# Kernel tuning notes

Hardware: AMD Instinct MI355X
Metric: run time of the kernel (lower is better)

Reference implementation:

```python
import jax, jax.numpy as jnp
import numpy as np

N = 2_000_000
REL_DIM = 14
CAN_DIM = 64
N_TYPES = 4


def setup_inputs() -> dict:
    key = jax.random.key(0)
    ka, kb, kia, kib, kw, kbias = jax.random.split(key, 6)
    return {
        "relation_logits_a": jax.random.normal(ka, (N, REL_DIM), dtype=jnp.float32),
        "relation_logits_b": jax.random.normal(kb, (N, REL_DIM), dtype=jnp.float32),
        "frame_type_ids_a": jax.random.randint(kia, (N,), 0, N_TYPES, dtype=jnp.int32),
        "frame_type_ids_b": jax.random.randint(kib, (N,), 0, N_TYPES, dtype=jnp.int32),
        # stacked expert params: W[e] is (REL_DIM, CAN_DIM), b[e] is (CAN_DIM,)
        "W": jax.random.normal(kw, (N_TYPES, REL_DIM, CAN_DIM), dtype=jnp.float32) * 0.26,
        "b": jax.random.normal(kbias, (N_TYPES, CAN_DIM), dtype=jnp.float32) * 0.26,
    }


def _batch_project(x, ids, W, b):
    # x: (N, REL_DIM), ids: (N,) int in [0, N_TYPES)
    # Masked dispatch to 4 tiny linear experts; peak intermediate is (N, CAN_DIM).
    out = jnp.zeros((x.shape[0], CAN_DIM), dtype=x.dtype)
    for e in range(N_TYPES):
        y = x @ W[e] + b[e]                      # (N, CAN_DIM)
        out = out + jnp.where((ids == e)[:, None], y, jnp.zeros((), x.dtype))
    return out


def reference(relation_logits_a, relation_logits_b, frame_type_ids_a, frame_type_ids_b, W, b):
    proj_a = _batch_project(relation_logits_a, frame_type_ids_a, W, b)
    proj_b = _batch_project(relation_logits_b, frame_type_ids_b, W, b)
    # F.mse_loss default reduction='mean'
    diff = proj_a - proj_b
    return jnp.mean(diff * diff)
```

## Files before the change

kernel.cpp:

```cpp
#include <hip/hip_runtime.h>
#include <hip/hip_bf16.h>
#include <hip/hip_fp16.h>


#define N_ROWS   2000000
#define CHUNK    64
#define N_CHUNKS (N_ROWS / CHUNK)
#define LDSP     72

typedef _Float16       h8  __attribute__((ext_vector_type(8)));
typedef float          f4  __attribute__((ext_vector_type(4)));
typedef unsigned short us8 __attribute__((ext_vector_type(8)));

__device__ __forceinline__ unsigned short f2h_bits(float x) {
    return __builtin_bit_cast(unsigned short, (_Float16)x);
}

__global__ void __launch_bounds__(64)
frame_loss_mfma(const float* __restrict__ A, const float* __restrict__ B,
                const int* __restrict__ IDA, const int* __restrict__ IDB,
                const float* __restrict__ W, const float* __restrict__ BIAS,
                float* __restrict__ out)
{
    __shared__ unsigned short sA[CHUNK * LDSP];
    __shared__ unsigned short sB[CHUNK * LDSP];

    const int lane = threadIdx.x & 63;
    const int sub  = lane & 15;
    const int quad = lane >> 4;

    h8 wf[8], nwf[8];
#pragma unroll
    for (int ct = 0; ct < 4; ++ct) {
#pragma unroll
        for (int s = 0; s < 2; ++s) {
            const int c = ct * 16 + sub;
            us8 bits;
#pragma unroll
            for (int j = 0; j < 8; ++j) {
                const int k = s * 32 + quad * 8 + j;
                float v = 0.0f;
                if (k < 56) {
                    const int e = k / 14;
                    const int kk = k - e * 14;
                    v = W[(e * 14 + kk) * 64 + c];
                } else if (k < 60) {
                    v = BIAS[(k - 56) * 64 + c];
                }
                bits[j] = f2h_bits(v);
            }
            wf[ct * 2 + s] = __builtin_bit_cast(h8, bits);
            us8 nb = bits ^ (unsigned short)0x8000;
            nwf[ct * 2 + s] = __builtin_bit_cast(h8, nb);
        }
    }

    float lsum = 0.0f;
    unsigned int* const rowA32 = (unsigned int*)(sA + lane * LDSP);
    unsigned int* const rowB32 = (unsigned int*)(sB + lane * LDSP);

    for (int chunk = blockIdx.x; chunk < N_CHUNKS; chunk += gridDim.x) {
        const int row = chunk * CHUNK + lane;
        const float2* ap = (const float2*)(A + (size_t)row * 14);
        const float2* bp = (const float2*)(B + (size_t)row * 14);
        float2 av[7], bv[7];
#pragma unroll
        for (int t = 0; t < 7; ++t) av[t] = ap[t];
#pragma unroll
        for (int t = 0; t < 7; ++t) bv[t] = bp[t];
        const int ea = IDA[row];
        const int eb = IDB[row];

        const us8 z = {0, 0, 0, 0, 0, 0, 0, 0};
#pragma unroll
        for (int t = 0; t < 9; ++t) ((us8*)rowA32)[t] = z;
#pragma unroll
        for (int t = 0; t < 9; ++t) ((us8*)rowB32)[t] = z;

#pragma unroll
        for (int t = 0; t < 7; ++t)
            rowA32[7 * ea + t] = (unsigned)f2h_bits(av[t].x) | ((unsigned)f2h_bits(av[t].y) << 16);
        rowA32[28 + (ea >> 1)] = 0x3C00u << (16 * (ea & 1));
#pragma unroll
        for (int t = 0; t < 7; ++t)
            rowB32[7 * eb + t] = (unsigned)f2h_bits(bv[t].x) | ((unsigned)f2h_bits(bv[t].y) << 16);
        rowB32[28 + (eb >> 1)] = 0x3C00u << (16 * (eb & 1));

        __syncthreads();

#pragma unroll
        for (int t = 0; t < 4; ++t) {
            const unsigned short* fa = sA + (t * 16 + sub) * LDSP + quad * 8;
            const unsigned short* fb = sB + (t * 16 + sub) * LDSP + quad * 8;
            h8 a0 = __builtin_bit_cast(h8, *(const us8*)fa);
            h8 a1 = __builtin_bit_cast(h8, *(const us8*)(fa + 32));
            h8 b0 = __builtin_bit_cast(h8, *(const us8*)fb);
            h8 b1 = __builtin_bit_cast(h8, *(const us8*)(fb + 32));
#pragma unroll
            for (int ct = 0; ct < 4; ++ct) {
                f4 acc = {0.0f, 0.0f, 0.0f, 0.0f};
                acc = __builtin_amdgcn_mfma_f32_16x16x32_f16(a0, wf[ct * 2 + 0], acc, 0, 0, 0);
                acc = __builtin_amdgcn_mfma_f32_16x16x32_f16(a1, wf[ct * 2 + 1], acc, 0, 0, 0);
                acc = __builtin_amdgcn_mfma_f32_16x16x32_f16(b0, nwf[ct * 2 + 0], acc, 0, 0, 0);
                acc = __builtin_amdgcn_mfma_f32_16x16x32_f16(b1, nwf[ct * 2 + 1], acc, 0, 0, 0);
                lsum += acc[0] * acc[0] + acc[1] * acc[1] + acc[2] * acc[2] + acc[3] * acc[3];
            }
        }
        __syncthreads();
    }

#pragma unroll
    for (int off = 32; off > 0; off >>= 1)
        lsum += __shfl_down(lsum, off, 64);
    if (lane == 0)
        atomicAdd(out, lsum * (1.0f / 128000000.0f));
}

extern "C" void kernel_launch(void* const* d_in, const int* in_sizes, int n_in,
                              void* d_out, int out_size, void* d_ws, size_t ws_size,
                              hipStream_t stream) {
    const float* A    = (const float*)d_in[0];
    const float* B    = (const float*)d_in[1];
    const int*   IDA  = (const int*)d_in[2];
    const int*   IDB  = (const int*)d_in[3];
    const float* W    = (const float*)d_in[4];
    const float* BIAS = (const float*)d_in[5];
    float* out = (float*)d_out;

    hipMemsetAsync(out, 0, sizeof(float), stream);
    frame_loss_mfma<<<dim3(4096), dim3(64), 0, stream>>>(A, B, IDA, IDB, W, BIAS, out);
}
```

Measured before the change: 280.4 us.

## Build MFMA operands in registers and fuse A−B difference before projection

Replaces the LDS staging of one-hot expanded rows with a register-level construction. Each lane selects its K-slice based on whether the row's expert id matches its quad, and computes the fp16 difference of A and B inputs before the MFMA. This halves MFMA count, since the projection of the difference equals the difference of projections, and removes the per-chunk LDS writes and barriers. It also switches to 256-thread blocks with weights staged once through LDS, uses vectorized float4 loads, and converts with pkrtz. The fp16 subtraction with round-toward-zero conversion changes rounding slightly.

```diff
diff --git a/kernel.cpp b/kernel.cpp
--- a/kernel.cpp
+++ b/kernel.cpp
@@ -1,114 +1,139 @@
 #include <hip/hip_runtime.h>
-#include <hip/hip_bf16.h>
 #include <hip/hip_fp16.h>
 
 
-#define N_ROWS   2000000
-#define CHUNK    64
-#define N_CHUNKS (N_ROWS / CHUNK)
-#define LDSP     72
+#define N_ROWS  2000000
+#define N_TILES (N_ROWS / 16)
+#define N_PAIRS (N_TILES / 2)
+#define NBLK    3125
+#define NTHR    256
 
-typedef _Float16       h8  __attribute__((ext_vector_type(8)));
-typedef float          f4  __attribute__((ext_vector_type(4)));
-typedef unsigned short us8 __attribute__((ext_vector_type(8)));
+typedef _Float16     h2 __attribute__((ext_vector_type(2)));
+typedef _Float16     h8 __attribute__((ext_vector_type(8)));
+typedef float        f4 __attribute__((ext_vector_type(4)));
+typedef unsigned int u4 __attribute__((ext_vector_type(4)));
 
-__device__ __forceinline__ unsigned short f2h_bits(float x) {
-    return __builtin_bit_cast(unsigned short, (_Float16)x);
+__device__ __forceinline__ unsigned int pkrtz(float a, float b) {
+    return __builtin_bit_cast(unsigned int, __builtin_amdgcn_cvt_pkrtz(a, b));
+}
+__device__ __forceinline__ unsigned int hsub2(unsigned int a, unsigned int b) {
+    h2 r = __builtin_bit_cast(h2, a) - __builtin_bit_cast(h2, b);
+    return __builtin_bit_cast(unsigned int, r);
+}
+__device__ __forceinline__ float ldW(const float* W, const float* BIAS, int k, int c) {
+    if (k < 56) return W[k * 64 + c];
+    if (k < 60) return BIAS[(k - 56) * 64 + c];
+    return 0.0f;
 }
 
-__global__ void __launch_bounds__(64)
-frame_loss_mfma(const float* __restrict__ A, const float* __restrict__ B,
-                const int* __restrict__ IDA, const int* __restrict__ IDB,
-                const float* __restrict__ W, const float* __restrict__ BIAS,
-                float* __restrict__ out)
+__global__ void __launch_bounds__(NTHR)
+frame_loss(const float* __restrict__ A, const float* __restrict__ B,
+           const int* __restrict__ IDA, const int* __restrict__ IDB,
+           const float* __restrict__ W, const float* __restrict__ BIAS,
+           float* __restrict__ out)
 {
-    __shared__ unsigned short sA[CHUNK * LDSP];
-    __shared__ unsigned short sB[CHUNK * LDSP];
+    __shared__ alignas(16) unsigned int sW[2048];
 
-    const int lane = threadIdx.x & 63;
+    const int tid = threadIdx.x;
+
+#pragma unroll
+    for (int it = 0; it < 8; ++it) {
+        const int idx = tid + it * 256;
+        const int f = idx >> 8, l = (idx >> 2) & 63, d = idx & 3;
+        const int lsub = l & 15, lquad = l >> 4, ct = f >> 1, s = f & 1;
+        const int c = ct * 16 + lsub, sd = s * 4 + d;
+        const int k = (sd < 7) ? (14 * lquad + 2 * sd) : (56 + 2 * lquad);
+        h2 p;
+        p.x = (_Float16)ldW(W, BIAS, k, c);
+        p.y = (_Float16)ldW(W, BIAS, k + 1, c);
+        sW[idx] = __builtin_bit_cast(unsigned int, p);
+    }
+    __syncthreads();
+
+    const int lane = tid & 63;
     const int sub  = lane & 15;
     const int quad = lane >> 4;
 
-    h8 wf[8], nwf[8];
+    u4 wf[8];
 #pragma unroll
-    for (int ct = 0; ct < 4; ++ct) {
+    for (int f = 0; f < 8; ++f)
+        wf[f] = *(const u4*)&sW[f * 256 + lane * 4];
+
+    const int wave   = blockIdx.x * (NTHR / 64) + (tid >> 6);
+    const int nwaves = NBLK * (NTHR / 64);
+
+    float ls0 = 0.0f, ls1 = 0.0f;
+
+    for (int pr = wave; pr < N_PAIRS; pr += nwaves) {
+        const int base0 = pr * 32;
+
+        unsigned int pa[2][7], pb[2][7];
+        int ia[2], ib[2];
+
 #pragma unroll
-        for (int s = 0; s < 2; ++s) {
-            const int c = ct * 16 + sub;
-            us8 bits;
+        for (int u = 0; u < 2; ++u) {
+            const int row = base0 + u * 16 + sub;
+            const float* ra = A + (size_t)row * 14;
+            const float* rb = B + (size_t)row * 14;
+            float4 xa0 = *(const float4*)(ra);
+            float4 xa1 = *(const float4*)(ra + 4);
+            float4 xa2 = *(const float4*)(ra + 8);
+            float2 xa3 = *(const float2*)(ra + 12);
+            float4 xb0 = *(const float4*)(rb);
+            float4 xb1 = *(const float4*)(rb + 4);
+            float4 xb2 = *(const float4*)(rb + 8);
+            float2 xb3 = *(const float2*)(rb + 12);
+            ia[u] = IDA[row];
+            ib[u] = IDB[row];
+            pa[u][0] = pkrtz(xa0.x, xa0.y); pa[u][1] = pkrtz(xa0.z, xa0.w);
+            pa[u][2] = pkrtz(xa1.x, xa1.y); pa[u][3] = pkrtz(xa1.z, xa1.w);
+            pa[u][4] = pkrtz(xa2.x, xa2.y); pa[u][5] = pkrtz(xa2.z, xa2.w);
+            pa[u][6] = pkrtz(xa3.x, xa3.y);
+            pb[u][0] = pkrtz(xb0.x, xb0.y); pb[u][1] = pkrtz(xb0.z, xb0.w);
+            pb[u][2] = pkrtz(xb1.x, xb1.y); pb[u][3] = pkrtz(xb1.z, xb1.w);
+            pb[u][4] = pkrtz(xb2.x, xb2.y); pb[u][5] = pkrtz(xb2.z, xb2.w);
+            pb[u][6] = pkrtz(xb3.x, xb3.y);
+        }
+
 #pragma unroll
-            for (int j = 0; j < 8; ++j) {
-                const int k = s * 32 + quad * 8 + j;
-                float v = 0.0f;
-                if (k < 56) {
-                    const int e = k / 14;
-                    const int kk = k - e * 14;
-                    v = W[(e * 14 + kk) * 64 + c];
-                } else if (k < 60) {
-                    v = BIAS[(k - 56) * 64 + c];
-                }
-                bits[j] = f2h_bits(v);
+        for (int u = 0; u < 2; ++u) {
+            const bool ma = (ia[u] == quad);
+            const bool mb = (ib[u] == quad);
+            unsigned int yd[8];
+#pragma unroll
+            for (int sd = 0; sd < 7; ++sd) {
+                const unsigned int va = ma ? pa[u][sd] : 0u;
+                const unsigned int vb = mb ? pb[u][sd] : 0u;
+                yd[sd] = hsub2(va, vb);
             }
-            wf[ct * 2 + s] = __builtin_bit_cast(h8, bits);
-            us8 nb = bits ^ (unsigned short)0x8000;
-            nwf[ct * 2 + s] = __builtin_bit_cast(h8, nb);
+            const unsigned int ta = 0x3C00u << ((ia[u] & 1) << 4);
+            const unsigned int tb = 0x3C00u << ((ib[u] & 1) << 4);
+            const unsigned int va7 = (quad == (ia[u] >> 1)) ? ta : 0u;
+            const unsigned int vb7 = (quad == (ib[u] >> 1)) ? tb : 0u;
+            yd[7] = hsub2(va7, vb7);
+
+            u4 lo4; lo4.x = yd[0]; lo4.y = yd[1]; lo4.z = yd[2]; lo4.w = yd[3];
+            u4 hi4; hi4.x = yd[4]; hi4.y = yd[5]; hi4.z = yd[6]; hi4.w = yd[7];
+            const h8 e0 = __builtin_bit_cast(h8, lo4);
+            const h8 e1 = __builtin_bit_cast(h8, hi4);
+
+#pragma unroll
+            for (int ct = 0; ct < 4; ++ct) {
+                const f4 z = {0.0f, 0.0f, 0.0f, 0.0f};
+                f4 acc;
+                acc = __builtin_amdgcn_mfma_f32_16x16x32_f16(
+                          e0, __builtin_bit_cast(h8, wf[ct * 2 + 0]), z, 0, 0, 0);
+                acc = __builtin_amdgcn_mfma_f32_16x16x32_f16(
+                          e1, __builtin_bit_cast(h8, wf[ct * 2 + 1]), acc, 0, 0, 0);
+                ls0 = fmaf(acc[0], acc[0], ls0);
+                ls1 = fmaf(acc[1], acc[1], ls1);
+                ls0 = fmaf(acc[2], acc[2], ls0);
+                ls1 = fmaf(acc[3], acc[3], ls1);
+            }
         }
     }
 
-    float lsum = 0.0f;
-    unsigned int* const rowA32 = (unsigned int*)(sA + lane * LDSP);
-    unsigned int* const rowB32 = (unsigned int*)(sB + lane * LDSP);
-
-    for (int chunk = blockIdx.x; chunk < N_CHUNKS; chunk += gridDim.x) {
-        const int row = chunk * CHUNK + lane;
-        const float2* ap = (const float2*)(A + (size_t)row * 14);
-        const float2* bp = (const float2*)(B + (size_t)row * 14);
-        float2 av[7], bv[7];
-#pragma unroll
-        for (int t = 0; t < 7; ++t) av[t] = ap[t];
-#pragma unroll
-        for (int t = 0; t < 7; ++t) bv[t] = bp[t];
-        const int ea = IDA[row];
-        const int eb = IDB[row];
-
-        const us8 z = {0, 0, 0, 0, 0, 0, 0, 0};
-#pragma unroll
-        for (int t = 0; t < 9; ++t) ((us8*)rowA32)[t] = z;
-#pragma unroll
-        for (int t = 0; t < 9; ++t) ((us8*)rowB32)[t] = z;
-
-#pragma unroll
-        for (int t = 0; t < 7; ++t)
-            rowA32[7 * ea + t] = (unsigned)f2h_bits(av[t].x) | ((unsigned)f2h_bits(av[t].y) << 16);
-        rowA32[28 + (ea >> 1)] = 0x3C00u << (16 * (ea & 1));
-#pragma unroll
-        for (int t = 0; t < 7; ++t)
-            rowB32[7 * eb + t] = (unsigned)f2h_bits(bv[t].x) | ((unsigned)f2h_bits(bv[t].y) << 16);
-        rowB32[28 + (eb >> 1)] = 0x3C00u << (16 * (eb & 1));
-
-        __syncthreads();
-
-#pragma unroll
-        for (int t = 0; t < 4; ++t) {
-            const unsigned short* fa = sA + (t * 16 + sub) * LDSP + quad * 8;
-            const unsigned short* fb = sB + (t * 16 + sub) * LDSP + quad * 8;
-            h8 a0 = __builtin_bit_cast(h8, *(const us8*)fa);
-            h8 a1 = __builtin_bit_cast(h8, *(const us8*)(fa + 32));
-            h8 b0 = __builtin_bit_cast(h8, *(const us8*)fb);
-            h8 b1 = __builtin_bit_cast(h8, *(const us8*)(fb + 32));
-#pragma unroll
-            for (int ct = 0; ct < 4; ++ct) {
-                f4 acc = {0.0f, 0.0f, 0.0f, 0.0f};
-                acc = __builtin_amdgcn_mfma_f32_16x16x32_f16(a0, wf[ct * 2 + 0], acc, 0, 0, 0);
-                acc = __builtin_amdgcn_mfma_f32_16x16x32_f16(a1, wf[ct * 2 + 1], acc, 0, 0, 0);
-                acc = __builtin_amdgcn_mfma_f32_16x16x32_f16(b0, nwf[ct * 2 + 0], acc, 0, 0, 0);
-                acc = __builtin_amdgcn_mfma_f32_16x16x32_f16(b1, nwf[ct * 2 + 1], acc, 0, 0, 0);
-                lsum += acc[0] * acc[0] + acc[1] * acc[1] + acc[2] * acc[2] + acc[3] * acc[3];
-            }
-        }
-        __syncthreads();
-    }
-
+    float lsum = ls0 + ls1;
 #pragma unroll
     for (int off = 32; off > 0; off >>= 1)
         lsum += __shfl_down(lsum, off, 64);
@@ -128,5 +153,5 @@
     float* out = (float*)d_out;
 
     hipMemsetAsync(out, 0, sizeof(float), stream);
-    frame_loss_mfma<<<dim3(4096), dim3(64), 0, stream>>>(A, B, IDA, IDB, W, BIAS, out);
+    frame_loss<<<dim3(NBLK), dim3(NTHR), 0, stream>>>(A, B, IDA, IDB, W, BIAS, out);
 }
```

After: 357.5 us. +27.5%, slower.

## Fold A/B into one signed MFMA operand and double-buffer LDS with register prefetch

Applied to the files above, without the earlier changes.

Each row's A and negated B logits are packed into a single fp16 LDS row, with subtraction when both rows share an expert. This halves the MFMA count and LDS traffic and removes the negated weight copy. The main loop now prefetches the next chunk into registers while the current chunk is computed from one of two ping-pong LDS buffers. It drops the barriers, relying on each block being a single wave. Loads become float4, conversion uses packed RTZ conversion, the grid shrinks to 2048 blocks with occupancy hints, and the atomic is replaced by per-block partials plus a separate reduction kernel. RTZ rounding and the pre-subtraction change numerics slightly, and the barrier-free LDS reuse relies on single-wave ordering.

```diff
diff --git a/kernel.cpp b/kernel.cpp
--- a/kernel.cpp
+++ b/kernel.cpp
@@ -1,119 +1,179 @@
 #include <hip/hip_runtime.h>
-#include <hip/hip_bf16.h>
 #include <hip/hip_fp16.h>
 
 
 #define N_ROWS   2000000
-#define CHUNK    64
-#define N_CHUNKS (N_ROWS / CHUNK)
-#define LDSP     72
+#define N_CHUNKS (N_ROWS / 64)
+#define NBLK     2048
+#define LDSW     36
 
-typedef _Float16       h8  __attribute__((ext_vector_type(8)));
-typedef float          f4  __attribute__((ext_vector_type(4)));
-typedef unsigned short us8 __attribute__((ext_vector_type(8)));
+typedef _Float16     h8 __attribute__((ext_vector_type(8)));
+typedef float        f4 __attribute__((ext_vector_type(4)));
+typedef unsigned int u4 __attribute__((ext_vector_type(4)));
 
-__device__ __forceinline__ unsigned short f2h_bits(float x) {
-    return __builtin_bit_cast(unsigned short, (_Float16)x);
+__device__ __forceinline__ unsigned int pkrtz(float a, float b) {
+    return __builtin_bit_cast(unsigned int, __builtin_amdgcn_cvt_pkrtz(a, b));
 }
 
-__global__ void __launch_bounds__(64)
-frame_loss_mfma(const float* __restrict__ A, const float* __restrict__ B,
-                const int* __restrict__ IDA, const int* __restrict__ IDB,
-                const float* __restrict__ W, const float* __restrict__ BIAS,
-                float* __restrict__ out)
+struct RowRegs {
+    float a[14], b[14];
+    int ea, eb;
+};
+
+__device__ __forceinline__ RowRegs load_chunk(int c, int lane,
+        const float* __restrict__ A, const float* __restrict__ B,
+        const int* __restrict__ IDA, const int* __restrict__ IDB) {
+    RowRegs r;
+    const int row = c * 64 + lane;
+    const float* ra = A + (size_t)row * 14;
+    const float* rb = B + (size_t)row * 14;
+    float4 a0 = *(const float4*)(ra + 0);
+    float4 a1 = *(const float4*)(ra + 4);
+    float4 a2 = *(const float4*)(ra + 8);
+    float2 a3 = *(const float2*)(ra + 12);
+    float4 b0 = *(const float4*)(rb + 0);
+    float4 b1 = *(const float4*)(rb + 4);
+    float4 b2 = *(const float4*)(rb + 8);
+    float2 b3 = *(const float2*)(rb + 12);
+    r.ea = IDA[row];
+    r.eb = IDB[row];
+    r.a[0]=a0.x; r.a[1]=a0.y; r.a[2]=a0.z; r.a[3]=a0.w;
+    r.a[4]=a1.x; r.a[5]=a1.y; r.a[6]=a1.z; r.a[7]=a1.w;
+    r.a[8]=a2.x; r.a[9]=a2.y; r.a[10]=a2.z; r.a[11]=a2.w;
+    r.a[12]=a3.x; r.a[13]=a3.y;
+    r.b[0]=b0.x; r.b[1]=b0.y; r.b[2]=b0.z; r.b[3]=b0.w;
+    r.b[4]=b1.x; r.b[5]=b1.y; r.b[6]=b1.z; r.b[7]=b1.w;
+    r.b[8]=b2.x; r.b[9]=b2.y; r.b[10]=b2.z; r.b[11]=b2.w;
+    r.b[12]=b3.x; r.b[13]=b3.y;
+    return r;
+}
+
+__device__ __forceinline__ void scatter_chunk(unsigned int* __restrict__ row32,
+                                              const RowRegs& r) {
+    const u4 z = {0u, 0u, 0u, 0u};
+#pragma unroll
+    for (int t = 0; t < 8; ++t) ((u4*)row32)[t] = z;
+    if (r.ea == r.eb) {
+#pragma unroll
+        for (int t = 0; t < 7; ++t)
+            row32[7 * r.ea + t] = pkrtz(r.a[2*t] - r.b[2*t], r.a[2*t+1] - r.b[2*t+1]);
+    } else {
+#pragma unroll
+        for (int t = 0; t < 7; ++t)
+            row32[7 * r.ea + t] = pkrtz(r.a[2*t], r.a[2*t+1]);
+#pragma unroll
+        for (int t = 0; t < 7; ++t)
+            row32[7 * r.eb + t] = pkrtz(-r.b[2*t], -r.b[2*t+1]);
+        const unsigned wa = 0x3C00u << ((r.ea & 1) * 16);
+        const unsigned wb = 0xBC00u << ((r.eb & 1) * 16);
+        const int ja = 28 + (r.ea >> 1), jb = 28 + (r.eb >> 1);
+        if (ja == jb) row32[ja] = wa | wb;
+        else { row32[ja] = wa; row32[jb] = wb; }
+    }
+}
+
+__device__ __forceinline__ void compute_chunk(const unsigned int* __restrict__ sbuf,
+                                              int sub, int quad, const h8* wf,
+                                              float* ls) {
+#pragma unroll
+    for (int t = 0; t < 4; ++t) {
+        const unsigned int* fr = sbuf + (t * 16 + sub) * LDSW + quad * 4;
+        u4 lo = *(const u4*)fr;
+        u4 hi = *(const u4*)(fr + 16);
+        const h8 e0 = __builtin_bit_cast(h8, lo);
+        const h8 e1 = __builtin_bit_cast(h8, hi);
+#pragma unroll
+        for (int ct = 0; ct < 4; ++ct) {
+            const f4 z = {0.0f, 0.0f, 0.0f, 0.0f};
+            f4 acc = __builtin_amdgcn_mfma_f32_16x16x32_f16(e0, wf[ct * 2 + 0], z, 0, 0, 0);
+            acc     = __builtin_amdgcn_mfma_f32_16x16x32_f16(e1, wf[ct * 2 + 1], acc, 0, 0, 0);
+#pragma unroll
+            for (int rr = 0; rr < 4; ++rr)
+                ls[rr] = fmaf(acc[rr], acc[rr], ls[rr]);
+        }
+    }
+}
+
+__global__ void __launch_bounds__(64, 2)
+frame_loss(const float* __restrict__ A, const float* __restrict__ B,
+           const int* __restrict__ IDA, const int* __restrict__ IDB,
+           const float* __restrict__ W, const float* __restrict__ BIAS,
+           float* __restrict__ ws)
 {
-    __shared__ unsigned short sA[CHUNK * LDSP];
-    __shared__ unsigned short sB[CHUNK * LDSP];
+    __shared__ alignas(16) unsigned int s0[64 * LDSW];
+    __shared__ alignas(16) unsigned int s1[64 * LDSW];
 
-    const int lane = threadIdx.x & 63;
+    const int lane = threadIdx.x;
     const int sub  = lane & 15;
     const int quad = lane >> 4;
 
-    h8 wf[8], nwf[8];
+    h8 wf[8];
 #pragma unroll
-    for (int ct = 0; ct < 4; ++ct) {
+    for (int ct = 0; ct < 4; ++ct)
 #pragma unroll
         for (int s = 0; s < 2; ++s) {
+            h8 f;
             const int c = ct * 16 + sub;
-            us8 bits;
 #pragma unroll
             for (int j = 0; j < 8; ++j) {
                 const int k = s * 32 + quad * 8 + j;
                 float v = 0.0f;
-                if (k < 56) {
-                    const int e = k / 14;
-                    const int kk = k - e * 14;
-                    v = W[(e * 14 + kk) * 64 + c];
-                } else if (k < 60) {
-                    v = BIAS[(k - 56) * 64 + c];
-                }
-                bits[j] = f2h_bits(v);
+                if (k < 56)       v = W[k * 64 + c];
+                else if (k < 60)  v = BIAS[(k - 56) * 64 + c];
+                f[j] = (_Float16)v;
             }
-            wf[ct * 2 + s] = __builtin_bit_cast(h8, bits);
-            us8 nb = bits ^ (unsigned short)0x8000;
-            nwf[ct * 2 + s] = __builtin_bit_cast(h8, nb);
+            wf[ct * 2 + s] = f;
         }
+
+    float ls[4] = {0.0f, 0.0f, 0.0f, 0.0f};
+    unsigned int* const myrow0 = s0 + lane * LDSW;
+    unsigned int* const myrow1 = s1 + lane * LDSW;
+
+    int c = blockIdx.x;
+    RowRegs rr = load_chunk(c, lane, A, B, IDA, IDB);
+    scatter_chunk(myrow0, rr);
+
+    while (true) {
+        int n = c + NBLK;
+        bool more = (n < N_CHUNKS);
+        if (more) rr = load_chunk(n, lane, A, B, IDA, IDB);
+        compute_chunk(s0, sub, quad, wf, ls);
+        if (!more) break;
+        scatter_chunk(myrow1, rr);
+        c = n;
+
+        n = c + NBLK;
+        more = (n < N_CHUNKS);
+        if (more) rr = load_chunk(n, lane, A, B, IDA, IDB);
+        compute_chunk(s1, sub, quad, wf, ls);
+        if (!more) break;
+        scatter_chunk(myrow0, rr);
+        c = n;
     }
 
-    float lsum = 0.0f;
-    unsigned int* const rowA32 = (unsigned int*)(sA + lane * LDSP);
-    unsigned int* const rowB32 = (unsigned int*)(sB + lane * LDSP);
-
-    for (int chunk = blockIdx.x; chunk < N_CHUNKS; chunk += gridDim.x) {
-        const int row = chunk * CHUNK + lane;
-        const float2* ap = (const float2*)(A + (size_t)row * 14);
-        const float2* bp = (const float2*)(B + (size_t)row * 14);
-        float2 av[7], bv[7];
-#pragma unroll
-        for (int t = 0; t < 7; ++t) av[t] = ap[t];
-#pragma unroll
-        for (int t = 0; t < 7; ++t) bv[t] = bp[t];
-        const int ea = IDA[row];
-        const int eb = IDB[row];
-
-        const us8 z = {0, 0, 0, 0, 0, 0, 0, 0};
-#pragma unroll
-        for (int t = 0; t < 9; ++t) ((us8*)rowA32)[t] = z;
-#pragma unroll
-        for (int t = 0; t < 9; ++t) ((us8*)rowB32)[t] = z;
-
-#pragma unroll
-        for (int t = 0; t < 7; ++t)
-            rowA32[7 * ea + t] = (unsigned)f2h_bits(av[t].x) | ((unsigned)f2h_bits(av[t].y) << 16);
-        rowA32[28 + (ea >> 1)] = 0x3C00u << (16 * (ea & 1));
-#pragma unroll
-        for (int t = 0; t < 7; ++t)
-            rowB32[7 * eb + t] = (unsigned)f2h_bits(bv[t].x) | ((unsigned)f2h_bits(bv[t].y) << 16);
-        rowB32[28 + (eb >> 1)] = 0x3C00u << (16 * (eb & 1));
-
-        __syncthreads();
-
-#pragma unroll
-        for (int t = 0; t < 4; ++t) {
-            const unsigned short* fa = sA + (t * 16 + sub) * LDSP + quad * 8;
-            const unsigned short* fb = sB + (t * 16 + sub) * LDSP + quad * 8;
-            h8 a0 = __builtin_bit_cast(h8, *(const us8*)fa);
-            h8 a1 = __builtin_bit_cast(h8, *(const us8*)(fa + 32));
-            h8 b0 = __builtin_bit_cast(h8, *(const us8*)fb);
-            h8 b1 = __builtin_bit_cast(h8, *(const us8*)(fb + 32));
-#pragma unroll
-            for (int ct = 0; ct < 4; ++ct) {
-                f4 acc = {0.0f, 0.0f, 0.0f, 0.0f};
-                acc = __builtin_amdgcn_mfma_f32_16x16x32_f16(a0, wf[ct * 2 + 0], acc, 0, 0, 0);
-                acc = __builtin_amdgcn_mfma_f32_16x16x32_f16(a1, wf[ct * 2 + 1], acc, 0, 0, 0);
-                acc = __builtin_amdgcn_mfma_f32_16x16x32_f16(b0, nwf[ct * 2 + 0], acc, 0, 0, 0);
-                acc = __builtin_amdgcn_mfma_f32_16x16x32_f16(b1, nwf[ct * 2 + 1], acc, 0, 0, 0);
-                lsum += acc[0] * acc[0] + acc[1] * acc[1] + acc[2] * acc[2] + acc[3] * acc[3];
-            }
-        }
-        __syncthreads();
-    }
-
+    float lsum = ls[0] + ls[1] + ls[2] + ls[3];
 #pragma unroll
     for (int off = 32; off > 0; off >>= 1)
         lsum += __shfl_down(lsum, off, 64);
     if (lane == 0)
-        atomicAdd(out, lsum * (1.0f / 128000000.0f));
+        ws[blockIdx.x] = lsum;
+}
+
+__global__ void __launch_bounds__(256)
+reduce_partials(const float* __restrict__ ws, float* __restrict__ out)
+{
+    const int tid = threadIdx.x;
+    float s = 0.0f;
+#pragma unroll
+    for (int i = tid; i < NBLK; i += 256) s += ws[i];
+#pragma unroll
+    for (int off = 32; off > 0; off >>= 1)
+        s += __shfl_down(s, off, 64);
+    __shared__ float tmp[4];
+    if ((tid & 63) == 0) tmp[tid >> 6] = s;
+    __syncthreads();
+    if (tid == 0)
+        out[0] = (tmp[0] + tmp[1] + tmp[2] + tmp[3]) * (1.0f / 128000000.0f);
 }
 
 extern "C" void kernel_launch(void* const* d_in, const int* in_sizes, int n_in,
@@ -125,8 +185,9 @@
     const int*   IDB  = (const int*)d_in[3];
     const float* W    = (const float*)d_in[4];
     const float* BIAS = (const float*)d_in[5];
+    float* ws  = (float*)d_ws;
     float* out = (float*)d_out;
 
-    hipMemsetAsync(out, 0, sizeof(float), stream);
-    frame_loss_mfma<<<dim3(4096), dim3(64), 0, stream>>>(A, B, IDA, IDB, W, BIAS, out);
+    frame_loss<<<dim3(NBLK), dim3(64), 0, stream>>>(A, B, IDA, IDB, W, BIAS, ws);
+    reduce_partials<<<dim3(1), dim3(256), 0, stream>>>(ws, out);
 }
```

After: 272.7 us. 2.7% less time.
